# Kernel tuning notes

Hardware: AMD Instinct MI355X
Metric: run time of the kernel (lower is better)

Reference implementation:

```python
import jax, jax.numpy as jnp
import numpy as np

B, T, HID = 2, 2048, 1024
H, DK, DV = 8, 128, 128      # num_heads, head_f_dim (key), head_i_dim (value)
LR = 128                     # gate low-rank dim
EPS = 1e-5


def setup_inputs() -> dict:
    key = jax.random.key(0)
    ks = jax.random.split(key, 8)
    def w(k, shape, fan_in):
        return jax.random.normal(k, shape, jnp.float32) / np.float32(np.sqrt(fan_in))
    return {
        "hidden_states": jax.random.normal(ks[0], (B, T, HID), jnp.float32),
        "Wq": w(ks[1], (HID, HID), HID),   # key_dim x hidden
        "Wk": w(ks[2], (HID, HID), HID),
        "Wv": w(ks[3], (HID, HID), HID),   # value_dim x hidden
        "Wg1": w(ks[4], (LR, HID), HID),   # low-rank gate down
        "Wg2": w(ks[5], (HID, LR), LR),    # low-rank gate up
        "g_norm_weight": jnp.ones((HID,), jnp.float32),
        "Wo": w(ks[6], (HID, HID), HID),
    }


def _lightnet_fwd(x, Wq, Wk, Wv, Wg1, Wg2, g_norm_weight, Wo):
    b, t, _ = x.shape
    q = jax.nn.silu(x @ Wq.T).reshape(b, t, H, DK)
    k = (x @ Wk.T).reshape(b, t, H, DK)
    v = (x @ Wv.T).reshape(b, t, H, DV)

    # LightNet gating: normalized keys via logcumsumexp over time
    z = jax.lax.cumlogsumexp(k, axis=1)                 # [b,t,h,dk]
    k = jnp.exp(k - z)                                  # exp-normalized keys
    g = jnp.concatenate([z[:, :1], z[:, :-1]], axis=1) - z  # <= 0; g[:,0]=0

    scale = DK ** -0.5

    # gated linear attention recurrence: S_t = exp(g_t) * S_{t-1} + k_t v_t^T
    def step(S, inp):
        qt, kt, vt, gt = inp                            # [b,h,dk],[b,h,dk],[b,h,dv],[b,h,dk]
        S = jnp.exp(gt)[..., None] * S + kt[..., None] * vt[..., None, :]
        o = jnp.einsum('bhk,bhkv->bhv', qt, S) * scale
        return S, o

    S0 = jnp.zeros((b, H, DK, DV), x.dtype)
    tfirst = lambda a: jnp.moveaxis(a, 1, 0)
    _, oT = jax.lax.scan(step, S0, (tfirst(q), tfirst(k), tfirst(v), tfirst(g)))
    o = jnp.moveaxis(oT, 0, 1).reshape(b, t, H * DV)    # [b,t,hidden]

    # RMSNorm(o) * swish(gate) then output projection
    gate = (x @ Wg1.T) @ Wg2.T
    o = o * jax.lax.rsqrt(jnp.mean(o * o, axis=-1, keepdims=True) + EPS) * g_norm_weight
    o = o * gate * jax.nn.sigmoid(gate)
    return o @ Wo.T


def reference(hidden_states, Wq, Wk, Wv, Wg1, Wg2, g_norm_weight, Wo):
    return _lightnet_fwd(hidden_states, Wq, Wk, Wv, Wg1, Wg2, g_norm_weight, Wo)
```

## Files before the change

kernel.cpp:

```cpp
#include <hip/hip_runtime.h>
#include <hip/hip_bf16.h>
#include <stdint.h>


typedef short short8 __attribute__((ext_vector_type(8)));
typedef float f32x4 __attribute__((ext_vector_type(4)));

#define T_SEQ 2048
#define HIDN  1024
#define SCALE 0.08838834764831845f
#define LDSP  136

__device__ __forceinline__ float blo(unsigned int u){
  union{unsigned int i; float f;} v; v.i = u << 16; return v.f;
}
__device__ __forceinline__ float bhi(unsigned int u){
  union{unsigned int i; float f;} v; v.i = u & 0xffff0000u; return v.f;
}
__device__ __forceinline__ float bu2f(unsigned short u){
  union{unsigned int i; float f;} v; v.i = ((unsigned int)u) << 16; return v.f;
}
__device__ __forceinline__ unsigned short f2bu(float f){
  union{float f; unsigned int i;} v; v.f = f;
  unsigned int x = v.i;
  x += 0x7fffu + ((x >> 16) & 1u);
  return (unsigned short)(x >> 16);
}
__device__ __forceinline__ void async16(const void* g, void* l){
  __builtin_amdgcn_global_load_lds(
      (const __attribute__((address_space(1))) unsigned int*)g,
      (__attribute__((address_space(3))) unsigned int*)l, 16, 0, 0);
}

__global__ __launch_bounds__(256) void convert_all(
    const float* __restrict__ X,  const float* __restrict__ Wq,
    const float* __restrict__ Wk, const float* __restrict__ Wv,
    const float* __restrict__ Wg1,const float* __restrict__ Wg2,
    const float* __restrict__ gnw,const float* __restrict__ Wo,
    unsigned short* __restrict__ base, float* __restrict__ SumSq)
{
  int q = blockIdx.x * 256 + threadIdx.x;
  const float* src; unsigned short* dst; int rel = q;
  if (rel < 1048576)            { src = X;   dst = base;            }
  else if ((rel -= 1048576) < 262144) { src = Wq;  dst = base + 4194304; }
  else if ((rel -=  262144) < 262144) { src = Wk;  dst = base + 5242880; }
  else if ((rel -=  262144) < 262144) { src = Wv;  dst = base + 6291456; }
  else if ((rel -=  262144) < 262144) { src = Wo;  dst = base + 7340032; }
  else if ((rel -=  262144) <  32768) { src = Wg1; dst = base + 8388608; }
  else if ((rel -=   32768) <  32768) { src = Wg2; dst = base + 8519680; }
  else if ((rel -=   32768) <    256) { src = gnw; dst = base + 8650752; }
  else { rel -= 256;
    ((float4*)SumSq)[rel] = make_float4(0.f,0.f,0.f,0.f); return; }
  float4 v = ((const float4*)src)[rel];
  ushort4 o; o.x=f2bu(v.x); o.y=f2bu(v.y); o.z=f2bu(v.z); o.w=f2bu(v.w);
  ((ushort4*)dst)[rel] = o;
}

__device__ __forceinline__ void gemm_core(
    const unsigned short* __restrict__ A, const unsigned short* __restrict__ B,
    int K, int row0, int col0,
    unsigned short* sA, unsigned short* sB, f32x4 acc[4][4], int tid)
{
  const int lane = tid & 63;
  const int wm = (tid >> 6) & 1, wn = tid >> 7;
  const int wb = tid & 192;
  for (int k0 = 0; k0 < K; k0 += 64){
    __syncthreads();
#pragma unroll
    for (int r = 0; r < 4; ++r){
      int idx  = r*256 + tid;
      int mrow = idx >> 3;
      int kc   = ((idx & 7) ^ (mrow & 7)) * 8;
      async16(A + (size_t)(row0 + mrow)*K + k0 + kc,
              sA + (size_t)(r*256 + wb)*8);
      async16(B + (size_t)(col0 + mrow)*K + k0 + kc,
              sB + (size_t)(r*256 + wb)*8);
    }
    __syncthreads();
#pragma unroll
    for (int h = 0; h < 2; ++h){
      short8 av[4], bv[4];
#pragma unroll
      for (int i=0;i<4;i++){
        int ra = wm*64 + i*16 + (lane&15);
        av[i] = *(const short8*)(sA + (size_t)ra*64
                                 + (((h*4 + (lane>>4)) ^ (ra & 7)) * 8));
      }
#pragma unroll
      for (int j=0;j<4;j++){
        int rb = wn*64 + j*16 + (lane&15);
        bv[j] = *(const short8*)(sB + (size_t)rb*64
                                 + (((h*4 + (lane>>4)) ^ (rb & 7)) * 8));
      }
#pragma unroll
      for (int i=0;i<4;i++)
#pragma unroll
        for (int j=0;j<4;j++)
          acc[i][j] = __builtin_amdgcn_mfma_f32_16x16x32_bf16(av[i], bv[j], acc[i][j], 0, 0, 0);
    }
  }
}

__device__ __forceinline__ void epilogue_lds(
    f32x4 acc[4][4], int row0, int col0, int tid, int ldc, int act,
    unsigned short* __restrict__ Cb, unsigned short* sC)
{
  const int lane = tid & 63;
  const int wm = (tid >> 6) & 1, wn = tid >> 7;
#pragma unroll
  for (int p=0;p<4;p++){
    __syncthreads();
    if (wm == (p>>1)){
#pragma unroll
      for (int ii=0; ii<2; ii++){
        int i = (p&1)*2 + ii;
        int lr = i*16 + ((lane>>4)<<2) - (p&1)*32;
#pragma unroll
        for (int j=0;j<4;j++){
          int col = wn*64 + j*16 + (lane&15);
#pragma unroll
          for (int r=0;r<4;r++){
            float v = acc[i][j][r];
            if (act == 1) v = v / (1.f + __expf(-v));
            else if (act == 2) v = __expf(v);
            sC[(lr+r)*128 + col] = f2bu(v);
          }
        }
      }
    }
    __syncthreads();
#pragma unroll
    for (int c = tid; c < 512; c += 256){
      int rr = c >> 4, off = (c & 15)*8;
      *(uint4*)&Cb[(size_t)(row0 + p*32 + rr)*ldc + col0 + off] =
          *(const uint4*)&sC[rr*128 + off];
    }
  }
}

__device__ __forceinline__ void epilogue_f32(
    f32x4 acc[4][4], int row0, int col0, int tid, int ldc,
    float* __restrict__ Cf)
{
  const int lane = tid & 63;
  const int wm = (tid >> 6) & 1, wn = tid >> 7;
#pragma unroll
  for (int i=0;i<4;i++){
    int rbase = row0 + wm*64 + i*16 + ((lane>>4)<<2);
#pragma unroll
    for (int j=0;j<4;j++){
      int col = col0 + wn*64 + j*16 + (lane&15);
#pragma unroll
      for (int r=0;r<4;r++)
        Cf[(size_t)(rbase + r)*ldc + col] = acc[i][j][r];
    }
  }
}

__global__ __launch_bounds__(256, 4) void proj_kernel(
    const unsigned short* __restrict__ X,
    const unsigned short* __restrict__ Wq, const unsigned short* __restrict__ Wk,
    const unsigned short* __restrict__ Wv, const unsigned short* __restrict__ Wg1,
    unsigned short* __restrict__ Qb, unsigned short* __restrict__ Eb,
    unsigned short* __restrict__ Vb, unsigned short* __restrict__ G1b)
{
  __shared__ unsigned short sA[128*64], sB[128*64];
  int tid = threadIdx.x;
  int which = blockIdx.y >> 3;
  const unsigned short* Bp = (which==0)?Wq:(which==1)?Wk:(which==2)?Wv:Wg1;
  int row0 = blockIdx.x * 128;
  int col0 = (which==3) ? 0 : (blockIdx.y & 7) * 128;
  f32x4 acc[4][4] = {};
  gemm_core(X, Bp, HIDN, row0, col0, sA, sB, acc, tid);
  if      (which==0) epilogue_lds(acc,row0,col0,tid,HIDN,1,Qb, sA);
  else if (which==1) epilogue_lds(acc,row0,col0,tid,HIDN,2,Eb, sA);
  else if (which==2) epilogue_lds(acc,row0,col0,tid,HIDN,0,Vb, sA);
  else               epilogue_lds(acc,row0,col0,tid,128 ,0,G1b,sA);
}

__global__ __launch_bounds__(256, 4) void gemm_bt(
    const unsigned short* __restrict__ A, const unsigned short* __restrict__ B,
    int K, int ldc, int act, float* __restrict__ Cf,
    unsigned short* __restrict__ Cb)
{
  __shared__ unsigned short sA[128*64], sB[128*64];
  int tid = threadIdx.x;
  int row0 = blockIdx.x * 128, col0 = blockIdx.y * 128;
  f32x4 acc[4][4] = {};
  gemm_core(A, B, K, row0, col0, sA, sB, acc, tid);
  if (Cb) epilogue_lds(acc, row0, col0, tid, ldc, act, Cb, sA);
  else    epilogue_f32(acc, row0, col0, tid, ldc, Cf);
}

__global__ __launch_bounds__(1024, 4) void attn_pass1(
    const unsigned short* __restrict__ Eb, const unsigned short* __restrict__ Vb,
    unsigned short* __restrict__ U, float* __restrict__ Esum)
{
  __shared__ unsigned short Vt[128*LDSP], Et[128*LDSP];
  __shared__ float seg_part[8*128];
  int tid = threadIdx.x;
  const int lane = tid & 63, quad = lane >> 4, l15 = lane & 15;
  const int w = tid >> 6;
  const int Rb = (w & 3)*32, Cb = (w >> 2)*32;
  int bh = blockIdx.x >> 4, ch = blockIdx.x & 15;
  int b = bh >> 3, h = bh & 7;
  size_t rowbase = (size_t)(b*T_SEQ + ch*128)*HIDN + h*128;

#pragma unroll
  for (int i=0;i<2;i++){
    int u = tid + i*1024; int t = u >> 4, kc = (u & 15)*8;
    int trot = (t + kc) & 127;
    unsigned short tmp[8];
    *(uint4*)tmp = *(const uint4*)&Vb[rowbase + (size_t)t*HIDN + kc];
#pragma unroll
    for (int j=0;j<8;j++) Vt[(kc+j)*LDSP + trot] = tmp[j];
    *(uint4*)tmp = *(const uint4*)&Eb[rowbase + (size_t)t*HIDN + kc];
#pragma unroll
    for (int j=0;j<8;j++) Et[(kc+j)*LDSP + trot] = tmp[j];
  }
  __syncthreads();

  {
    int seg = tid >> 7, k = tid & 127;
    float s = 0.f;
    for (int c = seg*16; c < seg*16+16; ++c)
      s += bu2f(Et[k*LDSP + ((c + (k & 120)) & 127)]);
    seg_part[seg*128 + k] = s;
  }
  __syncthreads();
  if (tid < 128){
    float s = 0.f;
#pragma unroll
    for (int ss=0; ss<8; ++ss) s += seg_part[ss*128 + tid];
    Esum[(size_t)blockIdx.x*128 + tid] = s;
  }

  f32x4 acc[2][2] = {};
#pragma unroll
  for (int s0=0; s0<128; s0+=32){
    short8 av[2], bv[2];
#pragma unroll
    for (int i=0;i<2;i++){
      int ra = Rb + i*16 + l15;
      av[i] = *(const short8*)(Vt + ra*LDSP + ((s0 + quad*8 + (ra & 120)) & 127));
    }
#pragma unroll
    for (int j=0;j<2;j++){
      int rb = Cb + j*16 + l15;
      bv[j] = *(const short8*)(Et + rb*LDSP + ((s0 + quad*8 + (rb & 120)) & 127));
    }
#pragma unroll
    for (int i=0;i<2;i++)
#pragma unroll
      for (int j=0;j<2;j++)
        acc[i][j] = __builtin_amdgcn_mfma_f32_16x16x32_bf16(av[i], bv[j], acc[i][j], 0,0,0);
  }
  __syncthreads();

#pragma unroll
  for (int i=0;i<2;i++)
#pragma unroll
    for (int j=0;j<2;j++){
      int k = Cb + j*16 + l15;
#pragma unroll
      for (int r=0;r<4;r++){
        int v = Rb + i*16 + quad*4 + r;
        Et[v*LDSP + k] = f2bu(acc[i][j][r]);
      }
    }
  __syncthreads();
  unsigned short* Ub = U + (size_t)blockIdx.x*16384;
#pragma unroll
  for (int i=0;i<2;i++){
    int u = tid + i*1024; int v = u >> 4, kc = (u & 15)*8;
    *(uint4*)&Ub[v*128 + kc] = *(const uint4*)&Et[v*LDSP + kc];
  }
}

__global__ __launch_bounds__(256) void attn_pass2(
    unsigned short* __restrict__ U, float* __restrict__ Esum)
{
  int bh = blockIdx.x >> 4, sl = blockIdx.x & 15;
  int p = sl*1024 + threadIdx.x*4;
  float r0=0.f, r1=0.f, r2=0.f, r3=0.f;
  for (int c=0;c<16;c++){
    ushort4* ptr = (ushort4*)&U[(size_t)(bh*16 + c)*16384 + p];
    ushort4 t = *ptr;
    ushort4 w;
    w.x=f2bu(r0); w.y=f2bu(r1); w.z=f2bu(r2); w.w=f2bu(r3);
    *ptr = w;
    r0 += bu2f(t.x); r1 += bu2f(t.y); r2 += bu2f(t.z); r3 += bu2f(t.w);
  }
  if (sl == 0 && threadIdx.x < 128){
    float r = 0.f;
    for (int c=0;c<16;c++){
      float* q = &Esum[(size_t)(bh*16 + c)*128 + threadIdx.x];
      float t = *q; *q = r; r += t;
    }
  }
}

__global__ __launch_bounds__(1024, 4) void attn_pass3(
    const unsigned short* __restrict__ Eb, const unsigned short* __restrict__ Qb,
    const unsigned short* __restrict__ Vb, const unsigned short* __restrict__ U,
    const float* __restrict__ Esum, unsigned short* __restrict__ Oatt,
    float* __restrict__ SumSq)
{
  __shared__ unsigned short bufA[128*LDSP];
  __shared__ unsigned short bufB[128*LDSP];
  __shared__ float seg_part[8*128];

  int tid = threadIdx.x;
  const int lane = tid & 63, quad = lane >> 4, l15 = lane & 15;
  const int w = tid >> 6;
  const int Rb = (w & 3)*32;
  const int Cbn = (w >> 2)*32;
  int bh = blockIdx.x >> 4, ch = blockIdx.x & 15;
  int b = bh >> 3, h = bh & 7;
  size_t rowbase = (size_t)(b*T_SEQ + ch*128)*HIDN + h*128;
  const unsigned short* Ublk = U + (size_t)blockIdx.x*16384;

#pragma unroll
  for (int i=0;i<2;i++){
    int u = tid + i*1024; int t = u >> 4, kc = (u & 15)*8;
    *(uint4*)&bufA[t*LDSP + kc] = *(const uint4*)&Qb[rowbase + (size_t)t*HIDN + kc];
    *(uint4*)&bufB[t*LDSP + kc] = *(const uint4*)&Eb[rowbase + (size_t)t*HIDN + kc];
  }
  __syncthreads();

  {
    int col = tid & 127, seg = tid >> 7;
    float psum = 0.f;
    for (int s = seg*16; s < seg*16+16; ++s) psum += bu2f(bufB[s*LDSP + col]);
    seg_part[seg*128 + col] = psum;
    __syncthreads();
    float run = Esum[(size_t)blockIdx.x*128 + col];
    for (int ss=0; ss<8; ++ss) if (ss < seg) run += seg_part[ss*128 + col];
    for (int s = seg*16; s < seg*16+16; ++s){
      run += bu2f(bufB[s*LDSP + col]);
      float q = bu2f(bufA[s*LDSP + col]);
      bufA[s*LDSP + col] = f2bu(q * SCALE * __builtin_amdgcn_rcpf(run));
    }
  }
  __syncthreads();

  f32x4 accO[2][2] = {}, accP[2][2] = {};
#pragma unroll
  for (int k0=0; k0<128; k0+=32){
    short8 av[2], bv[2];
#pragma unroll
    for (int i=0;i<2;i++)
      av[i] = *(const short8*)(bufA + (Rb + i*16 + l15)*LDSP + k0 + quad*8);
#pragma unroll
    for (int j=0;j<2;j++)
      bv[j] = *(const short8*)(Ublk + (size_t)(Cbn + j*16 + l15)*128 + k0 + quad*8);
#pragma unroll
    for (int i=0;i<2;i++)
#pragma unroll
      for (int j=0;j<2;j++)
        accO[i][j] = __builtin_amdgcn_mfma_f32_16x16x32_bf16(av[i], bv[j], accO[i][j], 0,0,0);
#pragma unroll
    for (int j=0;j<2;j++)
      bv[j] = *(const short8*)(bufB + (Cbn + j*16 + l15)*LDSP + k0 + quad*8);
#pragma unroll
    for (int i=0;i<2;i++)
#pragma unroll
      for (int j=0;j<2;j++)
        accP[i][j] = __builtin_amdgcn_mfma_f32_16x16x32_bf16(av[i], bv[j], accP[i][j], 0,0,0);
  }
  __syncthreads();

#pragma unroll
  for (int i=0;i<2;i++){
#pragma unroll
    for (int j=0;j<2;j++){
      int s = Cbn + j*16 + l15;
#pragma unroll
      for (int r=0;r<4;r++){
        int t = Rb + i*16 + quad*4 + r;
        bufA[t*LDSP + s] = f2bu(s <= t ? accP[i][j][r] : 0.f);
      }
    }
  }
#pragma unroll
  for (int i=0;i<2;i++){
    int u = tid + i*1024; int t = u >> 4, kc = (u & 15)*8;
    int trot = (t + kc) & 127;
    unsigned short tmp[8];
    *(uint4*)tmp = *(const uint4*)&Vb[rowbase + (size_t)t*HIDN + kc];
#pragma unroll
    for (int j=0;j<8;j++) bufB[(kc+j)*LDSP + trot] = tmp[j];
  }
  __syncthreads();

#pragma unroll
  for (int k0=0; k0<128; k0+=32){
    short8 av[2], bv[2];
#pragma unroll
    for (int i=0;i<2;i++)
      av[i] = *(const short8*)(bufA + (Rb + i*16 + l15)*LDSP + k0 + quad*8);
#pragma unroll
    for (int j=0;j<2;j++){
      int rv = Cbn + j*16 + l15;
      bv[j] = *(const short8*)(bufB + rv*LDSP + ((k0 + quad*8 + (rv & 120)) & 127));
    }
#pragma unroll
    for (int i=0;i<2;i++)
#pragma unroll
      for (int j=0;j<2;j++)
        accO[i][j] = __builtin_amdgcn_mfma_f32_16x16x32_bf16(av[i], bv[j], accO[i][j], 0,0,0);
  }
  __syncthreads();

#pragma unroll
  for (int i=0;i<2;i++){
#pragma unroll
    for (int j=0;j<2;j++){
      int vv = Cbn + j*16 + l15;
#pragma unroll
      for (int r=0;r<4;r++){
        int t = Rb + i*16 + quad*4 + r;
        bufA[t*LDSP + vv] = f2bu(accO[i][j][r]);
      }
    }
  }
  __syncthreads();

  {
    int seg = tid >> 7, row = tid & 127;
    float s = 0.f;
    for (int c = seg*16; c < seg*16+16; ++c){
      float x = bu2f(bufA[row*LDSP + c]); s += x*x;
    }
    seg_part[seg*128 + row] = s;
  }
#pragma unroll
  for (int i=0;i<2;i++){
    int u = tid + i*1024; int t = u >> 4, kc = (u & 15)*8;
    *(uint4*)&Oatt[rowbase + (size_t)t*HIDN + kc] = *(const uint4*)&bufA[t*LDSP + kc];
  }
  __syncthreads();
  if (tid < 128){
    float s = 0.f;
#pragma unroll
    for (int ss=0; ss<8; ++ss) s += seg_part[ss*128 + tid];
    atomicAdd(&SumSq[(size_t)b*T_SEQ + ch*128 + tid], s);
  }
}

__global__ __launch_bounds__(256) void norm_gate2(
    const unsigned short* __restrict__ Oatt, const unsigned short* __restrict__ Gt,
    const unsigned short* __restrict__ gnw, const float* __restrict__ SumSq,
    unsigned short* __restrict__ Onorm)
{
  int row = blockIdx.x, tid = threadIdx.x;
  float rstd = rsqrtf(SumSq[row] * (1.f/1024.f) + 1e-5f);
  ushort4 o4 = *(const ushort4*)&Oatt[(size_t)row*HIDN + tid*4];
  ushort4 g4 = *(const ushort4*)&Gt  [(size_t)row*HIDN + tid*4];
  ushort4 w4 = *(const ushort4*)&gnw[tid*4];
  ushort4 r4;
  r4.x = f2bu(bu2f(o4.x) * rstd * bu2f(w4.x) * bu2f(g4.x));
  r4.y = f2bu(bu2f(o4.y) * rstd * bu2f(w4.y) * bu2f(g4.y));
  r4.z = f2bu(bu2f(o4.z) * rstd * bu2f(w4.z) * bu2f(g4.z));
  r4.w = f2bu(bu2f(o4.w) * rstd * bu2f(w4.w) * bu2f(g4.w));
  *(ushort4*)&Onorm[(size_t)row*HIDN + tid*4] = r4;
}

extern "C" void kernel_launch(void* const* d_in, const int* in_sizes, int n_in,
                              void* d_out, int out_size, void* d_ws, size_t ws_size,
                              hipStream_t stream) {
  unsigned short* wsS = (unsigned short*)d_ws;

  unsigned short* Xc   = wsS;
  unsigned short* Wqc  = wsS + 4194304;
  unsigned short* Wkc  = wsS + 5242880;
  unsigned short* Wvc  = wsS + 6291456;
  unsigned short* Woc  = wsS + 7340032;
  unsigned short* Wg1c = wsS + 8388608;
  unsigned short* Wg2c = wsS + 8519680;
  unsigned short* gnwc = wsS + 8650752;
  unsigned short* Qb   = wsS + 8651776;
  unsigned short* Eb   = wsS + 12846080;
  unsigned short* Vb   = wsS + 17040384;
  unsigned short* G1b  = wsS + 21234688;
  unsigned short* Gt   = wsS + 21758976;
  unsigned short* Ub   = wsS + 25953280;
  unsigned short* Oattb= wsS + 30147584;
  float*          Esum = (float*)(wsS + 34341888);
  float*          SumSq= (float*)(wsS + 34407424);
  unsigned short* Onorm = Qb;

  convert_all<<<8453, 256, 0, stream>>>(
      (const float*)d_in[0], (const float*)d_in[1], (const float*)d_in[2],
      (const float*)d_in[3], (const float*)d_in[4], (const float*)d_in[5],
      (const float*)d_in[6], (const float*)d_in[7], wsS, SumSq);

  proj_kernel<<<dim3(32,25), 256, 0, stream>>>(Xc, Wqc, Wkc, Wvc, Wg1c, Qb, Eb, Vb, G1b);
  gemm_bt   <<<dim3(32,8),  256, 0, stream>>>(G1b, Wg2c, 128, HIDN, 1, nullptr, Gt);
  attn_pass1<<<256, 1024, 0, stream>>>(Eb, Vb, Ub, Esum);
  attn_pass2<<<256, 256, 0, stream>>>(Ub, Esum);
  attn_pass3<<<256, 1024, 0, stream>>>(Eb, Qb, Vb, Ub, Esum, Oattb, SumSq);
  norm_gate2<<<4096, 256, 0, stream>>>(Oattb, Gt, gnwc, SumSq, Onorm);
  gemm_bt   <<<dim3(32,8),  256, 0, stream>>>(Onorm, Woc, HIDN, HIDN, 0,
                                              (float*)d_out, nullptr);
}
```

Baseline: 188.0 us.

## Store V transposed from projection epilogue and use 128x64 GEMM tiles

The V projection epilogue now writes V transposed per (batch, head) into a [v][t] layout. This lets attn_pass1 and attn_pass3 load V tiles with async global-to-LDS copies in a XOR-swizzled layout, replacing the per-element transpose scatter into LDS. A new 128x64-tile GEMM (gemm_bt64) replaces the 128x128 one for the gate-up and output projections, doubling the block count for better CU occupancy. Launch bounds on the attention kernels are relaxed to 2 blocks per CU. The transposed V epilogue writes 8-byte strided chunks, which may be less coalesced.

After: 186.4 us. About the same (-0.8%).

```diff
diff --git a/kernel.cpp b/kernel.cpp
--- a/kernel.cpp
+++ b/kernel.cpp
@@ -11,12 +11,6 @@
 #define SCALE 0.08838834764831845f
 #define LDSP  136
 
-__device__ __forceinline__ float blo(unsigned int u){
-  union{unsigned int i; float f;} v; v.i = u << 16; return v.f;
-}
-__device__ __forceinline__ float bhi(unsigned int u){
-  union{unsigned int i; float f;} v; v.i = u & 0xffff0000u; return v.f;
-}
 __device__ __forceinline__ float bu2f(unsigned short u){
   union{unsigned int i; float f;} v; v.i = ((unsigned int)u) << 16; return v.f;
 }
@@ -157,12 +151,34 @@
   }
 }
 
+__device__ __forceinline__ void epilogue_vt(
+    f32x4 acc[4][4], int row0, int col0, int tid,
+    unsigned short* __restrict__ VT)
+{
+  const int lane = tid & 63, quad = lane >> 4, l15 = lane & 15;
+  const int wm = (tid >> 6) & 1, wn = tid >> 7;
+  size_t vtbase = ((size_t)(row0 >> 11)*8 + (col0 >> 7))*128;
+  int trow0 = row0 & 2047;
+#pragma unroll
+  for (int i=0;i<4;i++){
+    int t = trow0 + wm*64 + i*16 + quad*4;
+#pragma unroll
+    for (int j=0;j<4;j++){
+      int v = wn*64 + j*16 + l15;
+      ushort4 o;
+      o.x = f2bu(acc[i][j][0]); o.y = f2bu(acc[i][j][1]);
+      o.z = f2bu(acc[i][j][2]); o.w = f2bu(acc[i][j][3]);
+      *(ushort4*)&VT[(vtbase + v)*2048 + t] = o;
+    }
+  }
+}
+
 __global__ __launch_bounds__(256, 4) void proj_kernel(
     const unsigned short* __restrict__ X,
     const unsigned short* __restrict__ Wq, const unsigned short* __restrict__ Wk,
     const unsigned short* __restrict__ Wv, const unsigned short* __restrict__ Wg1,
     unsigned short* __restrict__ Qb, unsigned short* __restrict__ Eb,
-    unsigned short* __restrict__ Vb, unsigned short* __restrict__ G1b)
+    unsigned short* __restrict__ VT, unsigned short* __restrict__ G1b)
 {
   __shared__ unsigned short sA[128*64], sB[128*64];
   int tid = threadIdx.x;
@@ -174,7 +190,7 @@
   gemm_core(X, Bp, HIDN, row0, col0, sA, sB, acc, tid);
   if      (which==0) epilogue_lds(acc,row0,col0,tid,HIDN,1,Qb, sA);
   else if (which==1) epilogue_lds(acc,row0,col0,tid,HIDN,2,Eb, sA);
-  else if (which==2) epilogue_lds(acc,row0,col0,tid,HIDN,0,Vb, sA);
+  else if (which==2) epilogue_vt (acc,row0,col0,tid,VT);
   else               epilogue_lds(acc,row0,col0,tid,128 ,0,G1b,sA);
 }
 
@@ -192,11 +208,120 @@
   else    epilogue_f32(acc, row0, col0, tid, ldc, Cf);
 }
 
-__global__ __launch_bounds__(1024, 4) void attn_pass1(
-    const unsigned short* __restrict__ Eb, const unsigned short* __restrict__ Vb,
+__device__ __forceinline__ void gemm_core64(
+    const unsigned short* __restrict__ A, const unsigned short* __restrict__ B,
+    int K, int row0, int col0,
+    unsigned short* sA, unsigned short* sB, f32x4 acc[4][2], int tid)
+{
+  const int lane = tid & 63, quad = lane >> 4, l15 = lane & 15;
+  const int wm = (tid >> 6) & 1, wn = tid >> 7;
+  const int wb = tid & 192;
+  for (int k0 = 0; k0 < K; k0 += 64){
+    __syncthreads();
+#pragma unroll
+    for (int r = 0; r < 4; ++r){
+      int idx  = r*256 + tid;
+      int mrow = idx >> 3;
+      int kc   = ((idx & 7) ^ (mrow & 7)) * 8;
+      async16(A + (size_t)(row0 + mrow)*K + k0 + kc,
+              sA + (size_t)(r*256 + wb)*8);
+    }
+#pragma unroll
+    for (int r = 0; r < 2; ++r){
+      int idx  = r*256 + tid;
+      int brow = idx >> 3;
+      int kc   = ((idx & 7) ^ (brow & 7)) * 8;
+      async16(B + (size_t)(col0 + brow)*K + k0 + kc,
+              sB + (size_t)(r*256 + wb)*8);
+    }
+    __syncthreads();
+#pragma unroll
+    for (int h = 0; h < 2; ++h){
+      short8 av[4], bv[2];
+#pragma unroll
+      for (int i=0;i<4;i++){
+        int ra = wm*64 + i*16 + l15;
+        av[i] = *(const short8*)(sA + (size_t)ra*64
+                                 + (((h*4 + quad) ^ (ra & 7)) * 8));
+      }
+#pragma unroll
+      for (int j=0;j<2;j++){
+        int rb = wn*32 + j*16 + l15;
+        bv[j] = *(const short8*)(sB + (size_t)rb*64
+                                 + (((h*4 + quad) ^ (rb & 7)) * 8));
+      }
+#pragma unroll
+      for (int i=0;i<4;i++)
+#pragma unroll
+        for (int j=0;j<2;j++)
+          acc[i][j] = __builtin_amdgcn_mfma_f32_16x16x32_bf16(av[i], bv[j], acc[i][j], 0, 0, 0);
+    }
+  }
+}
+
+__global__ __launch_bounds__(256, 4) void gemm_bt64(
+    const unsigned short* __restrict__ A, const unsigned short* __restrict__ B,
+    int K, int ldc, int act, float* __restrict__ Cf,
+    unsigned short* __restrict__ Cb)
+{
+  __shared__ unsigned short sA[128*64], sB[64*64];
+  int tid = threadIdx.x;
+  const int lane = tid & 63, quad = lane >> 4, l15 = lane & 15;
+  const int wm = (tid >> 6) & 1, wn = tid >> 7;
+  int row0 = blockIdx.x * 128, col0 = blockIdx.y * 64;
+  f32x4 acc[4][2] = {};
+  gemm_core64(A, B, K, row0, col0, sA, sB, acc, tid);
+  if (Cb){
+    unsigned short* sC = sA;
+#pragma unroll
+    for (int p=0;p<4;p++){
+      __syncthreads();
+      if (wm == (p>>1)){
+#pragma unroll
+        for (int ii=0; ii<2; ii++){
+          int i = (p&1)*2 + ii;
+          int lr = i*16 + quad*4 - (p&1)*32;
+#pragma unroll
+          for (int j=0;j<2;j++){
+            int col = wn*32 + j*16 + l15;
+#pragma unroll
+            for (int r=0;r<4;r++){
+              float v = acc[i][j][r];
+              if (act == 1) v = v / (1.f + __expf(-v));
+              else if (act == 2) v = __expf(v);
+              sC[(lr+r)*64 + col] = f2bu(v);
+            }
+          }
+        }
+      }
+      __syncthreads();
+      {
+        int rr = tid >> 3, off = (tid & 7)*8;
+        *(uint4*)&Cb[(size_t)(row0 + p*32 + rr)*ldc + col0 + off] =
+            *(const uint4*)&sC[rr*64 + off];
+      }
+    }
+  } else {
+#pragma unroll
+    for (int i=0;i<4;i++){
+      int rbase = row0 + wm*64 + i*16 + quad*4;
+#pragma unroll
+      for (int j=0;j<2;j++){
+        int col = col0 + wn*32 + j*16 + l15;
+#pragma unroll
+        for (int r=0;r<4;r++)
+          Cf[(size_t)(rbase + r)*ldc + col] = acc[i][j][r];
+      }
+    }
+  }
+}
+
+__global__ __launch_bounds__(1024, 2) void attn_pass1(
+    const unsigned short* __restrict__ Eb, const unsigned short* __restrict__ VT,
     unsigned short* __restrict__ U, float* __restrict__ Esum)
 {
-  __shared__ unsigned short Vt[128*LDSP], Et[128*LDSP];
+  __shared__ unsigned short Vt[128*128];
+  __shared__ unsigned short Et[128*LDSP];
   __shared__ float seg_part[8*128];
   int tid = threadIdx.x;
   const int lane = tid & 63, quad = lane >> 4, l15 = lane & 15;
@@ -205,15 +330,21 @@
   int bh = blockIdx.x >> 4, ch = blockIdx.x & 15;
   int b = bh >> 3, h = bh & 7;
   size_t rowbase = (size_t)(b*T_SEQ + ch*128)*HIDN + h*128;
-
+  const unsigned short* VTb = VT + (size_t)bh*128*2048 + ch*128;
+
+#pragma unroll
+  for (int it=0; it<2; ++it){
+    int slot = it*1024 + tid;
+    int vrow = slot >> 4, c = slot & 15;
+    int cs = (c & 8) | ((c & 7) ^ (vrow & 7));
+    async16(VTb + (size_t)vrow*2048 + cs*8,
+            Vt + (size_t)(it*1024 + (tid & 960))*8);
+  }
 #pragma unroll
   for (int i=0;i<2;i++){
     int u = tid + i*1024; int t = u >> 4, kc = (u & 15)*8;
     int trot = (t + kc) & 127;
     unsigned short tmp[8];
-    *(uint4*)tmp = *(const uint4*)&Vb[rowbase + (size_t)t*HIDN + kc];
-#pragma unroll
-    for (int j=0;j<8;j++) Vt[(kc+j)*LDSP + trot] = tmp[j];
     *(uint4*)tmp = *(const uint4*)&Eb[rowbase + (size_t)t*HIDN + kc];
 #pragma unroll
     for (int j=0;j<8;j++) Et[(kc+j)*LDSP + trot] = tmp[j];
@@ -242,7 +373,9 @@
 #pragma unroll
     for (int i=0;i<2;i++){
       int ra = Rb + i*16 + l15;
-      av[i] = *(const short8*)(Vt + ra*LDSP + ((s0 + quad*8 + (ra & 120)) & 127));
+      int ck = (s0>>3) + quad;
+      int cx = (ck & 8) | ((ck & 7) ^ (ra & 7));
+      av[i] = *(const short8*)(Vt + (size_t)ra*128 + cx*8);
     }
 #pragma unroll
     for (int j=0;j<2;j++){
@@ -300,9 +433,9 @@
   }
 }
 
-__global__ __launch_bounds__(1024, 4) void attn_pass3(
+__global__ __launch_bounds__(1024, 2) void attn_pass3(
     const unsigned short* __restrict__ Eb, const unsigned short* __restrict__ Qb,
-    const unsigned short* __restrict__ Vb, const unsigned short* __restrict__ U,
+    const unsigned short* __restrict__ VT, const unsigned short* __restrict__ U,
     const float* __restrict__ Esum, unsigned short* __restrict__ Oatt,
     float* __restrict__ SumSq)
 {
@@ -319,6 +452,7 @@
   int b = bh >> 3, h = bh & 7;
   size_t rowbase = (size_t)(b*T_SEQ + ch*128)*HIDN + h*128;
   const unsigned short* Ublk = U + (size_t)blockIdx.x*16384;
+  const unsigned short* VTb = VT + (size_t)bh*128*2048 + ch*128;
 
 #pragma unroll
   for (int i=0;i<2;i++){
@@ -371,6 +505,14 @@
   __syncthreads();
 
 #pragma unroll
+  for (int it=0; it<2; ++it){
+    int slot = it*1024 + tid;
+    int vrow = slot >> 4, c = slot & 15;
+    int cs = (c & 8) | ((c & 7) ^ (vrow & 7));
+    async16(VTb + (size_t)vrow*2048 + cs*8,
+            bufB + (size_t)(it*1024 + (tid & 960))*8);
+  }
+#pragma unroll
   for (int i=0;i<2;i++){
 #pragma unroll
     for (int j=0;j<2;j++){
@@ -382,15 +524,6 @@
       }
     }
   }
-#pragma unroll
-  for (int i=0;i<2;i++){
-    int u = tid + i*1024; int t = u >> 4, kc = (u & 15)*8;
-    int trot = (t + kc) & 127;
-    unsigned short tmp[8];
-    *(uint4*)tmp = *(const uint4*)&Vb[rowbase + (size_t)t*HIDN + kc];
-#pragma unroll
-    for (int j=0;j<8;j++) bufB[(kc+j)*LDSP + trot] = tmp[j];
-  }
   __syncthreads();
 
 #pragma unroll
@@ -402,7 +535,9 @@
 #pragma unroll
     for (int j=0;j<2;j++){
       int rv = Cbn + j*16 + l15;
-      bv[j] = *(const short8*)(bufB + rv*LDSP + ((k0 + quad*8 + (rv & 120)) & 127));
+      int ck = (k0>>3) + quad;
+      int cx = (ck & 8) | ((ck & 7) ^ (rv & 7));
+      bv[j] = *(const short8*)(bufB + (size_t)rv*128 + cx*8);
     }
 #pragma unroll
     for (int i=0;i<2;i++)
@@ -481,7 +616,7 @@
   unsigned short* gnwc = wsS + 8650752;
   unsigned short* Qb   = wsS + 8651776;
   unsigned short* Eb   = wsS + 12846080;
-  unsigned short* Vb   = wsS + 17040384;
+  unsigned short* VTb  = wsS + 17040384;
   unsigned short* G1b  = wsS + 21234688;
   unsigned short* Gt   = wsS + 21758976;
   unsigned short* Ub   = wsS + 25953280;
@@ -495,12 +630,12 @@
       (const float*)d_in[3], (const float*)d_in[4], (const float*)d_in[5],
       (const float*)d_in[6], (const float*)d_in[7], wsS, SumSq);
 
-  proj_kernel<<<dim3(32,25), 256, 0, stream>>>(Xc, Wqc, Wkc, Wvc, Wg1c, Qb, Eb, Vb, G1b);
-  gemm_bt   <<<dim3(32,8),  256, 0, stream>>>(G1b, Wg2c, 128, HIDN, 1, nullptr, Gt);
-  attn_pass1<<<256, 1024, 0, stream>>>(Eb, Vb, Ub, Esum);
+  proj_kernel<<<dim3(32,25), 256, 0, stream>>>(Xc, Wqc, Wkc, Wvc, Wg1c, Qb, Eb, VTb, G1b);
+  gemm_bt64 <<<dim3(32,16), 256, 0, stream>>>(G1b, Wg2c, 128, HIDN, 1, nullptr, Gt);
+  attn_pass1<<<256, 1024, 0, stream>>>(Eb, VTb, Ub, Esum);
   attn_pass2<<<256, 256, 0, stream>>>(Ub, Esum);
-  attn_pass3<<<256, 1024, 0, stream>>>(Eb, Qb, Vb, Ub, Esum, Oattb, SumSq);
+  attn_pass3<<<256, 1024, 0, stream>>>(Eb, Qb, VTb, Ub, Esum, Oattb, SumSq);
   norm_gate2<<<4096, 256, 0, stream>>>(Oattb, Gt, gnwc, SumSq, Onorm);
-  gemm_bt   <<<dim3(32,8),  256, 0, stream>>>(Onorm, Woc, HIDN, HIDN, 0,
+  gemm_bt64 <<<dim3(32,16), 256, 0, stream>>>(Onorm, Woc, HIDN, 1024, 0,
                                               (float*)d_out, nullptr);
 }
```
